# Kernel tuning notes

Measured on AMD Instinct MI355X. Metric: run time of the kernel, lower is better.

The kernel has to match this reference:

```python
import jax, jax.numpy as jnp
import numpy as np

EPS = 1e-5


def conv2d(x, w, b=None, stride=1, padding=0, dilation=1, groups=1):
    out = jax.lax.conv_general_dilated(
        x, w, (stride, stride), [(padding, padding), (padding, padding)],
        rhs_dilation=(dilation, dilation),
        dimension_numbers=('NCHW', 'OIHW', 'NCHW'),
        feature_group_count=groups)
    if b is not None:
        out = out + b[None, :, None, None]
    return out


def unfold3(x):
    # torch nn.Unfold(kernel=3, padding=1), kept as [b, c, 9, h, w]
    # (channel-major ordering c*9+k, k = row-major kernel index, matches torch)
    b, c, h, w = x.shape
    xp = jnp.pad(x, ((0, 0), (0, 0), (1, 1), (1, 1)))
    return jnp.stack([xp[:, :, i:i + h, j:j + w]
                      for i in range(3) for j in range(3)], axis=2)


def setup_inputs():
    B, C, O, H, W = 8, 64, 64, 128, 128
    key = jax.random.key(0)
    ks = jax.random.split(key, 16)
    s = 0.05
    rn = lambda k, shape: jax.random.normal(k, shape, jnp.float32) * s
    return {
        'x': jax.random.normal(ks[0], (B, C, H, W), jnp.float32),
        'cdcm_conv1_w': rn(ks[1], (C, C, 1, 1)),
        'cdcm_conv1_b': jnp.zeros((C,), jnp.float32),
        'cdcm_w5': rn(ks[2], (C, C, 3, 3)),
        'cdcm_w7': rn(ks[3], (C, C, 3, 3)),
        'cdcm_w9': rn(ks[4], (C, C, 3, 3)),
        'cdcm_w11': rn(ks[5], (C, C, 3, 3)),
        'dsc_dw_w': rn(ks[6], (C, 1, 3, 3)),
        'dsc_dw_b': jnp.zeros((C,), jnp.float32),
        'dsc_pw_w': rn(ks[7], (C, C, 1, 1)),
        'dsc_pw_b': jnp.zeros((C,), jnp.float32),
        'gw_w': rn(ks[8], (C, 9, 9)),
        'gw_b': jnp.zeros((C, 9), jnp.float32),
        'gw_bn_g': jnp.ones((C, 9), jnp.float32),
        'gw_bn_b': jnp.zeros((C, 9), jnp.float32),
        'gw_bn_m': jnp.zeros((C, 9), jnp.float32),
        'gw_bn_v': jnp.ones((C, 9), jnp.float32),
        'conv_w': rn(ks[9], (O, C, 3, 3)),
        'conv_b': jnp.zeros((O,), jnp.float32),
        'fr_w': rn(ks[10], (O, O, 1, 1)),
        'fr_b': jnp.zeros((O,), jnp.float32),
        'ens_w': rn(ks[11], (3, O, O, 3, 3)),
        'ens_b': jnp.zeros((3, O), jnp.float32),
        'bn_g': jnp.ones((O,), jnp.float32),
        'bn_b': jnp.zeros((O,), jnp.float32),
        'bn_m': jnp.zeros((O,), jnp.float32),
        'bn_v': jnp.ones((O,), jnp.float32),
    }


def reference(x, cdcm_conv1_w, cdcm_conv1_b, cdcm_w5, cdcm_w7, cdcm_w9, cdcm_w11,
              dsc_dw_w, dsc_dw_b, dsc_pw_w, dsc_pw_b,
              gw_w, gw_b, gw_bn_g, gw_bn_b, gw_bn_m, gw_bn_v,
              conv_w, conv_b, fr_w, fr_b, ens_w, ens_b,
              bn_g, bn_b, bn_m, bn_v):
    C = x.shape[1]
    # ---- CDCM: relu -> 1x1 conv -> 4 dilated 3x3 convs, each through the
    # SAME DepthwiseSeparableConv instance, then summed ----
    y = conv2d(jax.nn.relu(x), cdcm_conv1_w, cdcm_conv1_b)

    def dsc(z):
        z = conv2d(z, dsc_dw_w, dsc_dw_b, padding=1, groups=C)
        return conv2d(z, dsc_pw_w, dsc_pw_b)

    y = sum(dsc(conv2d(y, w, padding=d, dilation=d))
            for w, d in ((cdcm_w5, 5), (cdcm_w7, 7), (cdcm_w9, 9), (cdcm_w11, 11)))

    b, c, h, w = y.shape
    patches = unfold3(y)  # [b, c, 9, h, w]

    # ---- dynamic weight generation: grouped 1x1 conv (groups=c, 9->9 per
    # group) + inference BatchNorm over the c*9 channels + softmax over the 9
    # patch positions ----
    gw = jnp.einsum('coi,bcihw->bcohw', gw_w, patches) + gw_b[None, :, :, None, None]
    scale = (gw_bn_g / jnp.sqrt(gw_bn_v + EPS))[None, :, :, None, None]
    gw = (gw - gw_bn_m[None, :, :, None, None]) * scale + gw_bn_b[None, :, :, None, None]
    wsm = jax.nn.softmax(gw, axis=2)

    # ---- involution core: the rearrange to (3h,3w) + stride-3 3x3 conv is
    # exactly a contraction of (patches * weights) with the conv kernel over
    # the 9 kernel positions (row-major kernel index == patch index) ----
    prod = patches * wsm  # [b, c, 9, h, w]
    O = conv_w.shape[0]
    out = jnp.einsum('bckhw,ock->bohw', prod, conv_w.reshape(O, c, 9)) + conv_b[None, :, None, None]

    # ---- feature reuse: conv1x1(conv_out) + conv_out ----
    out = conv2d(out, fr_w, fr_b) + out

    # ---- ensemble: mean of 3 conv3x3 ----
    out = jnp.mean(jnp.stack([conv2d(out, ens_w[i], ens_b[i], padding=1)
                              for i in range(3)]), axis=0)

    # ---- final BN (inference) + ReLU ----
    out = (out - bn_m[None, :, None, None]) * (bn_g / jnp.sqrt(bn_v + EPS))[None, :, None, None] \
          + bn_b[None, :, None, None]
    return jax.nn.relu(out)
```

## Files before the change

kernel.cpp:

```cpp
#include <hip/hip_runtime.h>
#include <hip/hip_bf16.h>
#include <hip/hip_fp16.h>

#define EPSV 1e-5f
#define Bn 8
#define Cn 64
#define Hn 128
#define Wn 128
#define Pn (Hn*Wn)
#define PR 150
#define PE 130
#define YPAD_ELEMS (Bn*PR*PR*Cn)

typedef _Float16 v8h __attribute__((ext_vector_type(8)));
typedef float v16f __attribute__((ext_vector_type(16)));
typedef unsigned short ushort8v __attribute__((ext_vector_type(8)));
typedef unsigned short ushort4v __attribute__((ext_vector_type(4)));

__device__ __forceinline__ unsigned short f2h(float v) {
  _Float16 h = (_Float16)v;
  return *reinterpret_cast<const unsigned short*>(&h);
}
__device__ __forceinline__ float h2f(unsigned short u) {
  return (float)(*reinterpret_cast<const _Float16*>(&u));
}

__device__ __forceinline__ v8h exp8h(v8h x) {
  union { v8h v; __half2 h[4]; } u; u.v = x;
  #pragma unroll
  for (int i = 0; i < 4; i++) u.h[i] = h2exp(u.h[i]);
  return u.v;
}
__device__ __forceinline__ v8h rcp8h(v8h x) {
  union { v8h v; __half2 h[4]; } u; u.v = x;
  #pragma unroll
  for (int i = 0; i < 4; i++) u.h[i] = h2rcp(u.h[i]);
  return u.v;
}

__device__ __forceinline__ size_t clb(int b, int row, int kb, int col, int PD) {
  return ((((size_t)b * PD + row) * 4 + kb) * PD + col) * 16;
}

__device__ __forceinline__ void swz_bh(int& b, int& h) {
  int bid = blockIdx.x;
  int w = (bid & 7) * 128 + (bid >> 3);
  b = w >> 7; h = w & 127;
}

__global__ __launch_bounds__(256) void k_prep(
    const float* __restrict__ w1, const float* __restrict__ w5,
    const float* __restrict__ w7, const float* __restrict__ w9,
    const float* __restrict__ w11, const float* __restrict__ pww,
    const float* __restrict__ frw, const float* __restrict__ cw,
    const float* __restrict__ gww, const float* __restrict__ gwb,
    const float* __restrict__ gbg, const float* __restrict__ gbb,
    const float* __restrict__ gbm, const float* __restrict__ gbv,
    const float* __restrict__ ensw, const float* __restrict__ ensb,
    const float* __restrict__ bng, const float* __restrict__ bnb,
    const float* __restrict__ bnm, const float* __restrict__ bnv,
    unsigned short* __restrict__ apack, unsigned short* __restrict__ apinv,
    unsigned short* __restrict__ apens, unsigned short* __restrict__ appw1,
    unsigned short* __restrict__ appw, unsigned short* __restrict__ apfr,
    unsigned short* __restrict__ gwpk,
    unsigned short* __restrict__ apk, unsigned short* __restrict__ bpk,
    float* __restrict__ esc, float* __restrict__ ebi,
    unsigned short* __restrict__ ypad, unsigned short* __restrict__ spad)
{
  int id = blockIdx.x * 256 + threadIdx.x;
  if (id < 147456) {
    int e = id & 7, l = (id >> 3) & 63, mh = (id >> 9) & 1,
        kbl = (id >> 10) & 1;
    int r2 = id >> 11;
    int t9 = r2 % 9; int dk = r2 / 9;
    int kbp = dk & 1, d = dk >> 1;
    int m = mh * 32 + (l & 31);
    int c = (kbp * 2 + kbl) * 16 + (l >> 5) * 8 + e;
    const float* src = (d == 0) ? w5 : (d == 1) ? w7 : (d == 2) ? w9 : w11;
    apack[id] = f2h(src[(m * 64 + c) * 9 + t9]);
    return;
  }
  id -= 147456;
  if (id < 36864) {
    int e = id & 7, l = (id >> 3) & 63, mh = (id >> 9) & 1,
        kb = (id >> 10) & 3, tap = id >> 12;
    int m = mh * 32 + (l & 31);
    int c = kb * 16 + (l >> 5) * 8 + e;
    apinv[id] = f2h(cw[(m * 64 + c) * 9 + tap]);
    return;
  }
  id -= 36864;
  if (id < 36864) {
    int e = id & 7, l = (id >> 3) & 63, mh = (id >> 9) & 1,
        kb = (id >> 10) & 3, tap = id >> 12;
    int m = mh * 32 + (l & 31);
    int c = kb * 16 + (l >> 5) * 8 + e;
    float v = (ensw[((0 * 64 + m) * 64 + c) * 9 + tap] +
               ensw[((64 + m) * 64 + c) * 9 + tap] +
               ensw[((128 + m) * 64 + c) * 9 + tap]) * (1.f / 3.f);
    apens[id] = f2h(v);
    return;
  }
  id -= 36864;
  if (id < 4096) {
    int e = id & 7, l = (id >> 3) & 63, mh = (id >> 9) & 1, kb = (id >> 10) & 3;
    int m = mh * 32 + (l & 31);
    int c = kb * 16 + (l >> 5) * 8 + e;
    appw1[id] = f2h(w1[m * 64 + c]);
    return;
  }
  id -= 4096;
  if (id < 4096) {
    int e = id & 7, l = (id >> 3) & 63, mh = (id >> 9) & 1, kb = (id >> 10) & 3;
    int m = mh * 32 + (l & 31);
    int c = kb * 16 + (l >> 5) * 8 + e;
    appw[id] = f2h(pww[m * 64 + c]);
    return;
  }
  id -= 4096;
  if (id < 4096) {
    int e = id & 7, l = (id >> 3) & 63, mh = (id >> 9) & 1, kb = (id >> 10) & 3;
    int m = mh * 32 + (l & 31);
    int c = kb * 16 + (l >> 5) * 8 + e;
    apfr[id] = f2h(frw[m * 64 + c]);
    return;
  }
  id -= 4096;
  if (id < 5184) {
    int cblk = id / 648, r = id - cblk * 648;
    int tap = r >> 3, ch = r & 7;
    int c = cblk * 8 + ch;
    gwpk[id] = f2h(gww[c * 81 + tap]);
    return;
  }
  id -= 5184;
  if (id < 576) {
    int cblk = id / 72, r = id - cblk * 72;
    int o = r >> 3, ch = r & 7;
    int c = cblk * 8 + ch;
    float A = gbg[c * 9 + o] / sqrtf(gbv[c * 9 + o] + EPSV);
    apk[id] = f2h(A);
    return;
  }
  id -= 576;
  if (id < 576) {
    int cblk = id / 72, r = id - cblk * 72;
    int o = r >> 3, ch = r & 7;
    int c = cblk * 8 + ch;
    float A = gbg[c * 9 + o] / sqrtf(gbv[c * 9 + o] + EPSV);
    float B = (gwb[c * 9 + o] - gbm[c * 9 + o]) * A + gbb[c * 9 + o];
    bpk[id] = f2h(B);
    return;
  }
  id -= 576;
  if (id < 64) {
    float s = bng[id] / sqrtf(bnv[id] + EPSV);
    esc[id] = s;
    float bm = (ensb[id] + ensb[64 + id] + ensb[128 + id]) * (1.f / 3.f);
    ebi[id] = (bm - bnm[id]) * s + bnb[id];
    return;
  }
  id -= 64;
  ushort8v z = {0, 0, 0, 0, 0, 0, 0, 0};
  const int perY = 22 * PR + 128 * 22;
  if (id < perY * Bn) {
    int b = id / perY; int r = id - b * perY;
    int tb = 22 * PR;
    int row, col;
    if (r < tb) {
      int rr = r / PR; col = r - rr * PR;
      row = (rr < 11) ? rr : (rr + 128);
    } else {
      int r2 = r - tb;
      row = 11 + r2 / 22;
      int cc = r2 % 22;
      col = (cc < 11) ? cc : (cc + 128);
    }
    #pragma unroll
    for (int kb = 0; kb < 4; kb++) {
      unsigned short* p = ypad + clb(b, row, kb, col, PR);
      *(ushort8v*)p = z;
      *(ushort8v*)(p + 8) = z;
    }
    return;
  }
  id -= perY * Bn;
  const int perS = 2 * PE + 256;
  if (id < perS * Bn) {
    int b = id / perS; int r = id - b * perS;
    int tb = 2 * PE;
    int row, col;
    if (r < tb) {
      int rr = r / PE; col = r - rr * PE;
      row = (rr < 1) ? 0 : 129;
    } else {
      int r2 = r - tb;
      row = 1 + r2 / 2;
      col = (r2 & 1) ? 129 : 0;
    }
    #pragma unroll
    for (int kb = 0; kb < 4; kb++) {
      unsigned short* p = spad + clb(b, row, kb, col, PE);
      *(ushort8v*)p = z;
      *(ushort8v*)(p + 8) = z;
    }
  }
}

__global__ __launch_bounds__(256, 4) void k_pw1x(const float* __restrict__ x,
    const unsigned short* __restrict__ apw, const float* __restrict__ bias,
    unsigned short* __restrict__ ypad)
{
  int b, h; swz_bh(b, h);
  const int tid = threadIdx.x, wv = tid >> 6, l = tid & 63;
  const int ln31 = l & 31, g = l >> 5;
  const int px = wv * 32 + ln31;
  const float* xb = x + ((size_t)b * Cn) * Pn + h * Wn + px;
  v16f acc0, acc1;
  #pragma unroll
  for (int r = 0; r < 16; r++) { acc0[r] = 0.f; acc1[r] = 0.f; }
  const unsigned short* apl = apw + l * 8;
  #pragma unroll
  for (int kb = 0; kb < 4; kb++) {
    int c0 = kb * 16 + g * 8;
    v8h Bf;
    #pragma unroll
    for (int e = 0; e < 8; e++)
      Bf[e] = (_Float16)fmaxf(xb[(size_t)(c0 + e) * Pn], 0.f);
    v8h A0 = *(const v8h*)(apl + (kb * 2) * 512);
    v8h A1 = *(const v8h*)(apl + (kb * 2 + 1) * 512);
    acc0 = __builtin_amdgcn_mfma_f32_32x32x16_f16(A0, Bf, acc0, 0, 0, 0);
    acc1 = __builtin_amdgcn_mfma_f32_32x32x16_f16(A1, Bf, acc1, 0, 0, 0);
  }
  #pragma unroll
  for (int t = 0; t < 4; t++) {
    int c0 = 8 * t + 4 * g;
    int kb = c0 >> 4, sub = c0 & 15;
    ushort4v s0, s1;
    #pragma unroll
    for (int u = 0; u < 4; u++) {
      s0[u] = f2h(acc0[4 * t + u] + bias[c0 + u]);
      s1[u] = f2h(acc1[4 * t + u] + bias[c0 + u + 32]);
    }
    *(ushort4v*)(ypad + clb(b, h + 11, kb, px + 11, PR) + sub) = s0;
    *(ushort4v*)(ypad + clb(b, h + 11, kb + 2, px + 11, PR) + sub) = s1;
  }
}

__global__ __launch_bounds__(256, 4) void k_cdcm_mfma(
    const unsigned short* __restrict__ ypad,
    const unsigned short* __restrict__ apack,
    unsigned short* __restrict__ spad)
{
  __shared__ __align__(16) unsigned short Abuf[18432];
  int b, h; swz_bh(b, h);
  const int tid = threadIdx.x, wv = tid >> 6, l = tid & 63;
  const int ln31 = l & 31, g = l >> 5;

  v16f acc0, acc1;
  #pragma unroll
  for (int r = 0; r < 16; r++) { acc0[r] = 0.f; acc1[r] = 0.f; }

  const unsigned short* abl = Abuf + l * 8;

  for (int d = 0; d < 4; d++) {
    const int dil = 5 + 2 * d;
    for (int kbp = 0; kbp < 2; kbp++) {
      __syncthreads();
      {
        const ushort8v* src = (const ushort8v*)(apack + (d * 2 + kbp) * 18432);
        ushort8v* dst = (ushort8v*)Abuf;
        #pragma unroll
        for (int it = 0; it < 9; it++)
          dst[tid + it * 256] = src[tid + it * 256];
      }
      __syncthreads();
      #pragma unroll
      for (int ky = 0; ky < 3; ky++) {
        const int row = h + 11 + (ky - 1) * dil;
        #pragma unroll
        for (int kx = 0; kx < 3; kx++) {
          const int col = wv * 32 + ln31 + (kx - 1) * dil + 11;
          const int t9 = ky * 3 + kx;
          #pragma unroll
          for (int kbl = 0; kbl < 2; kbl++) {
            const int kb = kbp * 2 + kbl;
            v8h Bf = *(const v8h*)(ypad + clb(b, row, kb, col, PR) + g * 8);
            const unsigned short* ap = abl + (t9 * 2 + kbl) * 1024;
            v8h A0 = *(const v8h*)(ap);
            v8h A1 = *(const v8h*)(ap + 512);
            acc0 = __builtin_amdgcn_mfma_f32_32x32x16_f16(A0, Bf, acc0, 0, 0, 0);
            acc1 = __builtin_amdgcn_mfma_f32_32x32x16_f16(A1, Bf, acc1, 0, 0, 0);
          }
        }
      }
    }
  }
  const int px = wv * 32 + ln31;
  #pragma unroll
  for (int t = 0; t < 4; t++) {
    int c0 = 8 * t + 4 * g;
    int kb = c0 >> 4, sub = c0 & 15;
    ushort4v s0, s1;
    #pragma unroll
    for (int u = 0; u < 4; u++) {
      s0[u] = f2h(acc0[4 * t + u]);
      s1[u] = f2h(acc1[4 * t + u]);
    }
    *(ushort4v*)(spad + clb(b, h + 1, kb, px + 1, PE) + sub) = s0;
    *(ushort4v*)(spad + clb(b, h + 1, kb + 2, px + 1, PE) + sub) = s1;
  }
}

__global__ __launch_bounds__(256, 4) void k_dwpw_mfma(
    const unsigned short* __restrict__ spad,
    const float* __restrict__ dww, const float* __restrict__ dwb,
    const unsigned short* __restrict__ appw, const float* __restrict__ pwb,
    unsigned short* __restrict__ y2pad)
{
  __shared__ float wdw[576];
  __shared__ float bdw[64];
  const int tid = threadIdx.x;
  for (int t = tid; t < 576; t += 256) wdw[t] = dww[t];
  if (tid < 64) bdw[tid] = dwb[tid];
  __syncthreads();

  int b, h; swz_bh(b, h);

  ushort8v z = {0, 0, 0, 0, 0, 0, 0, 0};
  if (h == 0) {
    for (int px = tid; px < 260; px += 256) {
      int row = (px < 130) ? 0 : 129;
      int col = (px < 130) ? px : px - 130;
      #pragma unroll
      for (int kb = 0; kb < 4; kb++) {
        unsigned short* p = y2pad + clb(b, row, kb, col, PE);
        *(ushort8v*)p = z;
        *(ushort8v*)(p + 8) = z;
      }
    }
  } else if (h == 1) {
    int row = 1 + (tid & 127);
    int col = (tid >> 7) ? 129 : 0;
    #pragma unroll
    for (int kb = 0; kb < 4; kb++) {
      unsigned short* p = y2pad + clb(b, row, kb, col, PE);
      *(ushort8v*)p = z;
      *(ushort8v*)(p + 8) = z;
    }
  }

  const int wv = tid >> 6, l = tid & 63;
  const int ln31 = l & 31, g = l >> 5;
  const int w = wv * 32 + ln31;

  v16f acc0, acc1;
  #pragma unroll
  for (int r = 0; r < 16; r++) { acc0[r] = 0.f; acc1[r] = 0.f; }
  const unsigned short* apl = appw + l * 8;

  #pragma unroll
  for (int kb = 0; kb < 4; kb++) {
    const int c0 = kb * 16 + g * 8;
    v8h t[9];
    #pragma unroll
    for (int k = 0; k < 9; k++) {
      const int dy = k / 3 - 1, dx = k % 3 - 1;
      t[k] = *(const v8h*)(spad + clb(b, h + 1 + dy, kb, w + 1 + dx, PE) + g * 8);
    }
    v8h dvh;
    #pragma unroll
    for (int e = 0; e < 8; e++) {
      const int c = c0 + e;
      float a = 4.f * bdw[c];
      #pragma unroll
      for (int k = 0; k < 9; k++) a += wdw[c * 9 + k] * (float)t[k][e];
      dvh[e] = (_Float16)a;
    }
    v8h A0 = *(const v8h*)(apl + (kb * 2) * 512);
    v8h A1 = *(const v8h*)(apl + (kb * 2 + 1) * 512);
    acc0 = __builtin_amdgcn_mfma_f32_32x32x16_f16(A0, dvh, acc0, 0, 0, 0);
    acc1 = __builtin_amdgcn_mfma_f32_32x32x16_f16(A1, dvh, acc1, 0, 0, 0);
  }
  #pragma unroll
  for (int t = 0; t < 4; t++) {
    int c0 = 8 * t + 4 * g;
    int kb = c0 >> 4, sub = c0 & 15;
    ushort4v s0, s1;
    #pragma unroll
    for (int u = 0; u < 4; u++) {
      s0[u] = f2h(acc0[4 * t + u] + 4.f * pwb[c0 + u]);
      s1[u] = f2h(acc1[4 * t + u] + 4.f * pwb[c0 + u + 32]);
    }
    *(ushort4v*)(y2pad + clb(b, h + 1, kb, w + 1, PE) + sub) = s0;
    *(ushort4v*)(y2pad + clb(b, h + 1, kb + 2, w + 1, PE) + sub) = s1;
  }
}

__global__ __launch_bounds__(256, 3) void k_invol_mfma(
    const unsigned short* __restrict__ y2pad,
    const unsigned short* __restrict__ gwpk,
    const unsigned short* __restrict__ apk,
    const unsigned short* __restrict__ bpk,
    const unsigned short* __restrict__ apinv,
    const float* __restrict__ cbias,
    unsigned short* __restrict__ ipad)
{
  __shared__ __align__(16) unsigned short gws[5184];
  __shared__ __align__(16) unsigned short As[576];
  __shared__ __align__(16) unsigned short Bs[576];
  const int tid = threadIdx.x;
  for (int t = tid; t < 648; t += 256)
    ((ushort8v*)gws)[t] = ((const ushort8v*)gwpk)[t];
  if (tid < 72) {
    ((ushort8v*)As)[tid] = ((const ushort8v*)apk)[tid];
    ((ushort8v*)Bs)[tid] = ((const ushort8v*)bpk)[tid];
  }
  __syncthreads();

  int b, h; swz_bh(b, h);
  const int wv = tid >> 6, l = tid & 63;
  const int p32 = l & 31, g = l >> 5;
  const int w = wv * 32 + p32;

  v16f acc0, acc1;
  #pragma unroll
  for (int r = 0; r < 16; r++) { acc0[r] = 0.f; acc1[r] = 0.f; }

  for (int cb4 = 0; cb4 < 4; cb4++) {
    const int cblk = cb4 * 2 + g;
    const unsigned short* gwp = gws + cblk * 648;
    const unsigned short* Ap = As + cblk * 72;
    const unsigned short* Bp = Bs + cblk * 72;

    v8h pt[9];
    #pragma unroll
    for (int k = 0; k < 9; k++) {
      const int dy = k / 3 - 1, dx = k % 3 - 1;
      pt[k] = *(const v8h*)(y2pad + clb(b, h + 1 + dy, cb4, w + 1 + dx, PE) + g * 8);
    }
    v8h s[9];
    #pragma unroll
    for (int o = 0; o < 9; o++) {
      v8h a = (*(const v8h*)(gwp + o * 72)) * pt[0];
      #pragma unroll
      for (int i = 1; i < 9; i++)
        a += (*(const v8h*)(gwp + o * 72 + i * 8)) * pt[i];
      s[o] = a * (*(const v8h*)(Ap + o * 8)) + (*(const v8h*)(Bp + o * 8));
    }
    v8h esum = {0, 0, 0, 0, 0, 0, 0, 0};
    #pragma unroll
    for (int o = 0; o < 9; o++) { s[o] = exp8h(s[o]); esum += s[o]; }
    v8h inv = rcp8h(esum);
    #pragma unroll
    for (int k = 0; k < 9; k++) pt[k] = pt[k] * s[k] * inv;

    const unsigned short* ap = apinv + l * 8;
    #pragma unroll
    for (int k = 0; k < 9; k++) {
      const unsigned short* a2 = ap + ((k * 4 + cb4) * 2) * 512;
      v8h A0 = *(const v8h*)(a2);
      v8h A1 = *(const v8h*)(a2 + 512);
      acc0 = __builtin_amdgcn_mfma_f32_32x32x16_f16(A0, pt[k], acc0, 0, 0, 0);
      acc1 = __builtin_amdgcn_mfma_f32_32x32x16_f16(A1, pt[k], acc1, 0, 0, 0);
    }
  }
  #pragma unroll
  for (int t = 0; t < 4; t++) {
    int c0 = 8 * t + 4 * g;
    int kb = c0 >> 4, sub = c0 & 15;
    ushort4v s0, s1;
    #pragma unroll
    for (int u = 0; u < 4; u++) {
      s0[u] = f2h(acc0[4 * t + u] + cbias[c0 + u]);
      s1[u] = f2h(acc1[4 * t + u] + cbias[c0 + u + 32]);
    }
    *(ushort4v*)(ipad + clb(b, h, kb, w, 128) + sub) = s0;
    *(ushort4v*)(ipad + clb(b, h, kb + 2, w, 128) + sub) = s1;
  }
}

__global__ __launch_bounds__(256, 4) void k_fr_mfma(
    const unsigned short* __restrict__ ipad,
    const unsigned short* __restrict__ apfr,
    const float* __restrict__ bias,
    unsigned short* __restrict__ opad)
{
  int b, h; swz_bh(b, h);
  const int tid = threadIdx.x, wv = tid >> 6, l = tid & 63;
  const int ln31 = l & 31, g = l >> 5;
  const int px = wv * 32 + ln31;
  v16f acc0, acc1;
  #pragma unroll
  for (int r = 0; r < 16; r++) { acc0[r] = 0.f; acc1[r] = 0.f; }
  const unsigned short* apl = apfr + l * 8;
  #pragma unroll
  for (int kb = 0; kb < 4; kb++) {
    v8h Bf = *(const v8h*)(ipad + clb(b, h, kb, px, 128) + g * 8);
    v8h A0 = *(const v8h*)(apl + (kb * 2) * 512);
    v8h A1 = *(const v8h*)(apl + (kb * 2 + 1) * 512);
    acc0 = __builtin_amdgcn_mfma_f32_32x32x16_f16(A0, Bf, acc0, 0, 0, 0);
    acc1 = __builtin_amdgcn_mfma_f32_32x32x16_f16(A1, Bf, acc1, 0, 0, 0);
  }
  #pragma unroll
  for (int t = 0; t < 4; t++) {
    int c0 = 8 * t + 4 * g;
    int kb = c0 >> 4, sub = c0 & 15;
    ushort4v r0 = *(const ushort4v*)(ipad + clb(b, h, kb, px, 128) + sub);
    ushort4v r1 = *(const ushort4v*)(ipad + clb(b, h, kb + 2, px, 128) + sub);
    ushort4v s0, s1;
    #pragma unroll
    for (int u = 0; u < 4; u++) {
      s0[u] = f2h(acc0[4 * t + u] + bias[c0 + u] + h2f(r0[u]));
      s1[u] = f2h(acc1[4 * t + u] + bias[c0 + u + 32] + h2f(r1[u]));
    }
    *(ushort4v*)(opad + clb(b, h + 1, kb, px + 1, PE) + sub) = s0;
    *(ushort4v*)(opad + clb(b, h + 1, kb + 2, px + 1, PE) + sub) = s1;
  }
}

__global__ __launch_bounds__(256) void k_ens_mfma(
    const unsigned short* __restrict__ opad,
    const unsigned short* __restrict__ apens,
    const float* __restrict__ esc, const float* __restrict__ ebi,
    float* __restrict__ out)
{
  __shared__ __align__(16) unsigned short Abuf[36864];
  const int tid = threadIdx.x;
  {
    const ushort8v* src = (const ushort8v*)apens;
    ushort8v* dst = (ushort8v*)Abuf;
    #pragma unroll
    for (int it = 0; it < 18; it++)
      dst[tid + it * 256] = src[tid + it * 256];
  }
  __syncthreads();

  const int bid = blockIdx.x;
  const int b = bid & 7, h0 = (bid >> 3) * 2;
  const int wv = tid >> 6, l = tid & 63;
  const int ln31 = l & 31, g = l >> 5;

  v16f a00, a01, a10, a11;
  #pragma unroll
  for (int r = 0; r < 16; r++) { a00[r] = 0.f; a01[r] = 0.f; a10[r] = 0.f; a11[r] = 0.f; }

  const unsigned short* abl = Abuf + l * 8;

  #pragma unroll
  for (int ky = 0; ky < 3; ky++) {
    #pragma unroll
    for (int kx = 0; kx < 3; kx++) {
      const int tap = ky * 3 + kx;
      const int r0 = h0 + ky;
      const int col = wv * 32 + ln31 + kx;
      const unsigned short* ap = abl + tap * 4096;
      #pragma unroll
      for (int kb = 0; kb < 4; kb++) {
        v8h B0 = *(const v8h*)(opad + clb(b, r0, kb, col, PE) + g * 8);
        v8h B1 = *(const v8h*)(opad + clb(b, r0 + 1, kb, col, PE) + g * 8);
        v8h A0 = *(const v8h*)(ap + kb * 1024);
        v8h A1 = *(const v8h*)(ap + kb * 1024 + 512);
        a00 = __builtin_amdgcn_mfma_f32_32x32x16_f16(A0, B0, a00, 0, 0, 0);
        a01 = __builtin_amdgcn_mfma_f32_32x32x16_f16(A1, B0, a01, 0, 0, 0);
        a10 = __builtin_amdgcn_mfma_f32_32x32x16_f16(A0, B1, a10, 0, 0, 0);
        a11 = __builtin_amdgcn_mfma_f32_32x32x16_f16(A1, B1, a11, 0, 0, 0);
      }
    }
  }
  float* sp0 = out + ((size_t)b * Cn) * Pn + h0 * Wn + wv * 32 + ln31;
  float* sp1 = sp0 + Wn;
  #pragma unroll
  for (int r = 0; r < 16; r++) {
    int o0 = (r & 3) + 8 * (r >> 2) + 4 * g;
    float e0 = esc[o0], e1 = esc[o0 + 32];
    float i0 = ebi[o0], i1 = ebi[o0 + 32];
    sp0[(size_t)o0 * Pn] = fmaxf(a00[r] * e0 + i0, 0.f);
    sp0[(size_t)(o0 + 32) * Pn] = fmaxf(a01[r] * e1 + i1, 0.f);
    sp1[(size_t)o0 * Pn] = fmaxf(a10[r] * e0 + i0, 0.f);
    sp1[(size_t)(o0 + 32) * Pn] = fmaxf(a11[r] * e1 + i1, 0.f);
  }
}

extern "C" void kernel_launch(void* const* d_in, const int* in_sizes, int n_in,
                              void* d_out, int out_size, void* d_ws, size_t ws_size,
                              hipStream_t stream)
{
  const float* x    = (const float*)d_in[0];
  const float* w1   = (const float*)d_in[1];
  const float* b1   = (const float*)d_in[2];
  const float* w5   = (const float*)d_in[3];
  const float* w7   = (const float*)d_in[4];
  const float* w9   = (const float*)d_in[5];
  const float* w11  = (const float*)d_in[6];
  const float* dww  = (const float*)d_in[7];
  const float* dwb  = (const float*)d_in[8];
  const float* pww  = (const float*)d_in[9];
  const float* pwb  = (const float*)d_in[10];
  const float* gww  = (const float*)d_in[11];
  const float* gwb  = (const float*)d_in[12];
  const float* gbg  = (const float*)d_in[13];
  const float* gbb  = (const float*)d_in[14];
  const float* gbm  = (const float*)d_in[15];
  const float* gbv  = (const float*)d_in[16];
  const float* cw   = (const float*)d_in[17];
  const float* cb   = (const float*)d_in[18];
  const float* frw  = (const float*)d_in[19];
  const float* frb  = (const float*)d_in[20];
  const float* ensw = (const float*)d_in[21];
  const float* ensb = (const float*)d_in[22];
  const float* bng  = (const float*)d_in[23];
  const float* bnb  = (const float*)d_in[24];
  const float* bnm  = (const float*)d_in[25];
  const float* bnv  = (const float*)d_in[26];

  unsigned short* wsu   = (unsigned short*)d_ws;
  unsigned short* ypad  = wsu;
  unsigned short* y2pad = wsu;
  unsigned short* opad  = wsu;
  unsigned short* apack = wsu + YPAD_ELEMS;
  unsigned short* apinv = apack + 147456;
  unsigned short* apens = apinv + 36864;
  unsigned short* appw1 = apens + 36864;
  unsigned short* appw  = appw1 + 4096;
  unsigned short* apfr  = appw + 4096;
  unsigned short* gwpk  = apfr + 4096;
  unsigned short* apk   = gwpk + 5184;
  unsigned short* bpk   = apk + 576;
  float* esc = (float*)(bpk + 576);
  float* ebi = esc + 64;

  unsigned short* spad = (unsigned short*)d_out;
  unsigned short* ipad = (unsigned short*)d_out;
  float* D = (float*)d_out;

  k_prep<<<1145, 256, 0, stream>>>(w1, w5, w7, w9, w11, pww, frw, cw,
                                   gww, gwb, gbg, gbb, gbm, gbv, ensw, ensb,
                                   bng, bnb, bnm, bnv,
                                   apack, apinv, apens, appw1, appw, apfr,
                                   gwpk, apk, bpk, esc, ebi,
                                   ypad, spad);

  k_pw1x<<<1024, 256, 0, stream>>>(x, appw1, b1, ypad);
  k_cdcm_mfma<<<1024, 256, 0, stream>>>(ypad, apack, spad);
  k_dwpw_mfma<<<1024, 256, 0, stream>>>(spad, dww, dwb, appw, pwb, y2pad);
  k_invol_mfma<<<1024, 256, 0, stream>>>(y2pad, gwpk, apk, bpk, apinv, cb, ipad);
  k_fr_mfma<<<1024, 256, 0, stream>>>(ipad, apfr, frb, opad);
  k_ens_mfma<<<512, 256, 0, stream>>>(opad, apens, esc, ebi, D);
}
```

Before: 160.8 us.

## Double-buffer CDCM weights via async global-to-LDS loads and compute two rows per block

```diff
diff --git a/kernel.cpp b/kernel.cpp
--- a/kernel.cpp
+++ b/kernel.cpp
@@ -36,6 +36,12 @@
   #pragma unroll
   for (int i = 0; i < 4; i++) u.h[i] = h2rcp(u.h[i]);
   return u.v;
+}
+
+__device__ __forceinline__ void gload_lds16(const void* g, void* l) {
+  __builtin_amdgcn_global_load_lds(
+      (const __attribute__((address_space(1))) unsigned int*)g,
+      (__attribute__((address_space(3))) unsigned int*)l, 16, 0, 0);
 }
 
 __device__ __forceinline__ size_t clb(int b, int row, int kb, int col, int PD) {
@@ -247,37 +253,55 @@
   }
 }
 
-__global__ __launch_bounds__(256, 4) void k_cdcm_mfma(
+__global__ __launch_bounds__(256) void k_cdcm_mfma(
     const unsigned short* __restrict__ ypad,
     const unsigned short* __restrict__ apack,
     unsigned short* __restrict__ spad)
 {
-  __shared__ __align__(16) unsigned short Abuf[18432];
-  int b, h; swz_bh(b, h);
+  __shared__ __align__(16) unsigned short Abuf[2][18432];
+  const int bid = blockIdx.x;
+  const int b = bid & 7, h0 = (bid >> 3) * 2;
   const int tid = threadIdx.x, wv = tid >> 6, l = tid & 63;
   const int ln31 = l & 31, g = l >> 5;
 
-  v16f acc0, acc1;
-  #pragma unroll
-  for (int r = 0; r < 16; r++) { acc0[r] = 0.f; acc1[r] = 0.f; }
-
-  const unsigned short* abl = Abuf + l * 8;
-
+  {
+    const char* src = (const char*)apack;
+    char* dst = (char*)&Abuf[0][0];
+    #pragma unroll
+    for (int it = 0; it < 9; it++) {
+      int off = (wv * 9 + it) * 1024;
+      gload_lds16(src + off + l * 16, dst + off);
+    }
+  }
+
+  v16f a00, a01, a10, a11;
+  #pragma unroll
+  for (int r = 0; r < 16; r++) { a00[r] = 0.f; a01[r] = 0.f; a10[r] = 0.f; a11[r] = 0.f; }
+
+  #pragma unroll
   for (int d = 0; d < 4; d++) {
     const int dil = 5 + 2 * d;
+    #pragma unroll
     for (int kbp = 0; kbp < 2; kbp++) {
-      __syncthreads();
-      {
-        const ushort8v* src = (const ushort8v*)(apack + (d * 2 + kbp) * 18432);
-        ushort8v* dst = (ushort8v*)Abuf;
+      const int c = d * 2 + kbp;
+      if (c < 7) {
+        const char* src = (const char*)(apack + (c + 1) * 18432);
+        char* dst = (char*)&Abuf[(c + 1) & 1][0];
         #pragma unroll
-        for (int it = 0; it < 9; it++)
-          dst[tid + it * 256] = src[tid + it * 256];
+        for (int it = 0; it < 9; it++) {
+          int off = (wv * 9 + it) * 1024;
+          gload_lds16(src + off + l * 16, dst + off);
+        }
+        asm volatile("s_waitcnt vmcnt(9)" ::: "memory");
+      } else {
+        asm volatile("s_waitcnt vmcnt(0)" ::: "memory");
       }
-      __syncthreads();
+      asm volatile("s_barrier" ::: "memory");
+
+      const unsigned short* abl = &Abuf[c & 1][0] + l * 8;
       #pragma unroll
       for (int ky = 0; ky < 3; ky++) {
-        const int row = h + 11 + (ky - 1) * dil;
+        const int r0 = h0 + 11 + (ky - 1) * dil;
         #pragma unroll
         for (int kx = 0; kx < 3; kx++) {
           const int col = wv * 32 + ln31 + (kx - 1) * dil + 11;
@@ -285,15 +309,19 @@
           #pragma unroll
           for (int kbl = 0; kbl < 2; kbl++) {
             const int kb = kbp * 2 + kbl;
-            v8h Bf = *(const v8h*)(ypad + clb(b, row, kb, col, PR) + g * 8);
+            v8h B0 = *(const v8h*)(ypad + clb(b, r0, kb, col, PR) + g * 8);
+            v8h B1 = *(const v8h*)(ypad + clb(b, r0 + 1, kb, col, PR) + g * 8);
             const unsigned short* ap = abl + (t9 * 2 + kbl) * 1024;
             v8h A0 = *(const v8h*)(ap);
             v8h A1 = *(const v8h*)(ap + 512);
-            acc0 = __builtin_amdgcn_mfma_f32_32x32x16_f16(A0, Bf, acc0, 0, 0, 0);
-            acc1 = __builtin_amdgcn_mfma_f32_32x32x16_f16(A1, Bf, acc1, 0, 0, 0);
+            a00 = __builtin_amdgcn_mfma_f32_32x32x16_f16(A0, B0, a00, 0, 0, 0);
+            a01 = __builtin_amdgcn_mfma_f32_32x32x16_f16(A1, B0, a01, 0, 0, 0);
+            a10 = __builtin_amdgcn_mfma_f32_32x32x16_f16(A0, B1, a10, 0, 0, 0);
+            a11 = __builtin_amdgcn_mfma_f32_32x32x16_f16(A1, B1, a11, 0, 0, 0);
           }
         }
       }
+      asm volatile("s_barrier" ::: "memory");
     }
   }
   const int px = wv * 32 + ln31;
@@ -301,14 +329,18 @@
   for (int t = 0; t < 4; t++) {
     int c0 = 8 * t + 4 * g;
     int kb = c0 >> 4, sub = c0 & 15;
-    ushort4v s0, s1;
+    ushort4v s0, s1, s2, s3;
     #pragma unroll
     for (int u = 0; u < 4; u++) {
-      s0[u] = f2h(acc0[4 * t + u]);
-      s1[u] = f2h(acc1[4 * t + u]);
-    }
-    *(ushort4v*)(spad + clb(b, h + 1, kb, px + 1, PE) + sub) = s0;
-    *(ushort4v*)(spad + clb(b, h + 1, kb + 2, px + 1, PE) + sub) = s1;
+      s0[u] = f2h(a00[4 * t + u]);
+      s1[u] = f2h(a01[4 * t + u]);
+      s2[u] = f2h(a10[4 * t + u]);
+      s3[u] = f2h(a11[4 * t + u]);
+    }
+    *(ushort4v*)(spad + clb(b, h0 + 1, kb, px + 1, PE) + sub) = s0;
+    *(ushort4v*)(spad + clb(b, h0 + 1, kb + 2, px + 1, PE) + sub) = s1;
+    *(ushort4v*)(spad + clb(b, h0 + 2, kb, px + 1, PE) + sub) = s2;
+    *(ushort4v*)(spad + clb(b, h0 + 2, kb + 2, px + 1, PE) + sub) = s3;
   }
 }
 
@@ -642,7 +674,7 @@
                                    ypad, spad);
 
   k_pw1x<<<1024, 256, 0, stream>>>(x, appw1, b1, ypad);
-  k_cdcm_mfma<<<1024, 256, 0, stream>>>(ypad, apack, spad);
+  k_cdcm_mfma<<<512, 256, 0, stream>>>(ypad, apack, spad);
   k_dwpw_mfma<<<1024, 256, 0, stream>>>(spad, dww, dwb, appw, pwb, y2pad);
   k_invol_mfma<<<1024, 256, 0, stream>>>(y2pad, gwpk, apk, bpk, apinv, cb, ipad);
   k_fr_mfma<<<1024, 256, 0, stream>>>(ipad, apfr, frb, opad);
```

After: 150.0 us. 1.07x faster.
